# Kernel optimization log

Measured on AMD Instinct MI355X. Metric: run time of the kernel, lower is better.

## Reference

```python
import jax, jax.numpy as jnp
import numpy as np

B, C, N, K, CO = 16, 256, 16384, 64, 512
EPS_NORM = 1e-12
BN_EPS = 1e-5


def _l2norm(v, axis):
    n = jnp.sqrt(jnp.sum(v * v, axis=axis, keepdims=True))
    return v / jnp.maximum(n, EPS_NORM)


def setup_inputs() -> dict:
    key = jax.random.key(0)
    ks = jax.random.split(key, 8)
    x = jax.random.normal(ks[0], (B, C, N), dtype=jnp.float32)
    # NetVLAD assignment conv: Conv1d(C, K, k=1) -> weight (K, C), bias (K)
    assign_w = jax.random.normal(ks[1], (K, C), dtype=jnp.float32) / np.sqrt(C)
    assign_b = jax.random.normal(ks[2], (K,), dtype=jnp.float32) / np.sqrt(C)
    centroids = jax.random.uniform(ks[3], (K, C), dtype=jnp.float32)
    # reduct_feat Conv1d(K*C, CO, k=1): weight (CO, K*C), bias (CO)
    red_w = jax.random.normal(ks[4], (CO, K * C), dtype=jnp.float32) * np.sqrt(2.0 / (K * C))
    red_b = jnp.zeros((CO,), dtype=jnp.float32)
    bn_w = jnp.ones((CO,), dtype=jnp.float32)
    bn_b = jnp.zeros((CO,), dtype=jnp.float32)
    return {"x": x, "assign_w": assign_w, "assign_b": assign_b,
            "centroids": centroids, "red_w": red_w, "red_b": red_b,
            "bn_w": bn_w, "bn_b": bn_b}


def reference(x, assign_w, assign_b, centroids, red_w, red_b, bn_w, bn_b):
    # --- NetVLAD ---
    xn = _l2norm(x, axis=1)                                   # (B,C,N) L2 over channel
    logits = jnp.einsum('kc,bcn->bkn', assign_w, xn) + assign_b[None, :, None]
    a = jax.nn.softmax(logits, axis=1)                        # (B,K,N) soft assignment
    # residual aggregation reformulated: sum_n a*(x - c) = (a @ x^T) - sum_n(a) * c
    agg = jnp.einsum('bkn,bcn->bkc', a, xn)                   # (B,K,C)
    a_sum = jnp.sum(a, axis=2)                                # (B,K)
    vlad = agg - a_sum[:, :, None] * centroids[None, :, :]    # (B,K,C)
    vlad = _l2norm(vlad, axis=2)                              # intra-norm over C
    vlad = vlad.reshape(B, K * C)
    vlad = _l2norm(vlad, axis=1)                              # global L2
    # --- reduct_feat: 1x1 conv on length-1 sequence ---
    y = vlad @ red_w.T + red_b                                # (B,CO)
    # BatchNorm1d, training mode: stats over batch (L=1), biased variance
    mean = jnp.mean(y, axis=0)
    var = jnp.mean((y - mean) ** 2, axis=0)
    y = bn_w * (y - mean) / jnp.sqrt(var + BN_EPS) + bn_b
    y = jax.nn.relu(y)
    return y[:, :, None]                                      # (B,CO,1)
```

## Files before the change

### kernel.cpp

```cpp
#include <hip/hip_runtime.h>
#include <math.h>

#define B_   16
#define C_   256
#define N_   16384
#define K_   64
#define CO_  512

typedef __attribute__((ext_vector_type(8))) short short8;
typedef __attribute__((ext_vector_type(4))) short short4v;
typedef __attribute__((ext_vector_type(4))) float floatx4;

__device__ inline unsigned int f2bf(float f) {
    unsigned int u = __float_as_uint(f);
    return (u + 0x7FFFu + ((u >> 16) & 1u)) >> 16;
}


__global__ __launch_bounds__(512, 4) void k1_assign_agg(
    const float* __restrict__ x, const float* __restrict__ aw,
    const float* __restrict__ ab, float* __restrict__ agg,
    float* __restrict__ asum)
{
    __shared__ __align__(16) unsigned char smem[79872];
    unsigned short* x_cn = (unsigned short*)smem;
    unsigned short* x_nc = (unsigned short*)(smem + 32768);
    unsigned short* a_ld = (unsigned short*)(smem + 66048);
    float* colsq = (float*)(smem + 74240);
    float* rnorm = (float*)(smem + 78592);
    float* part  = (float*)(smem + 78848);
    float* red   = part;

    const int t    = threadIdx.x;
    const int lane = t & 63;
    const int wav  = t >> 6;
    const int b    = blockIdx.x >> 5;
    const int tile = blockIdx.x & 31;
    const float* xb = x + (size_t)b * ((size_t)C_ * N_) + tile * 512;

    const int j16 = lane & 15;
    const int g4  = lane >> 4;
    const int mw  = wav & 3;
    const int jw  = wav >> 2;
    const int p   = t & 31;
    const int g   = t >> 5;

    short8 wf[8];
    {
        const float* wrow = aw + (mw * 16 + j16) * 256 + g4 * 8;
        #pragma unroll
        for (int ki = 0; ki < 8; ++ki) {
            const float* q = wrow + ki * 32;
            short8 f;
            #pragma unroll
            for (int i = 0; i < 8; ++i) f[i] = (short)f2bf(q[i]);
            wf[ki] = f;
        }
    }
    const float4 abf = *(const float4*)(ab + mw * 16 + g4 * 4);

    floatx4 acc[4][2];
    #pragma unroll
    for (int m = 0; m < 4; ++m)
        #pragma unroll
        for (int c2 = 0; c2 < 2; ++c2)
            acc[m][c2] = (floatx4){0.f, 0.f, 0.f, 0.f};
    float asr[4] = {0.f, 0.f, 0.f, 0.f};

    float2 v[16];
    {
        const float* ps = xb + 2 * p;
        #pragma unroll
        for (int i = 0; i < 16; ++i)
            v[i] = *(const float2*)(ps + (size_t)(g * 16 + i) * N_);
    }

    for (int chunk = 0; chunk < 8; ++chunk) {
        __syncthreads();
        float sq0 = 0.f, sq1 = 0.f;
        #pragma unroll
        for (int half = 0; half < 2; ++half) {
            unsigned int hL[8], hH[8];
            #pragma unroll
            for (int i = 0; i < 8; ++i) {
                float2 vv = v[half * 8 + i];
                sq0 += vv.x * vv.x; sq1 += vv.y * vv.y;
                hL[i] = f2bf(vv.x); hH[i] = f2bf(vv.y);
                int c = g * 16 + half * 8 + i;
                ((unsigned int*)x_cn)[c * 32 + (((p >> 1) ^ (c & 14)) << 1) + (p & 1)]
                    = hL[i] | (hH[i] << 16);
            }
            unsigned short* r0 = x_nc + (2 * p) * 260 + g * 16 + half * 8;
            unsigned short* r1 = r0 + 260;
            uint2 wl0, wl1, wh0, wh1;
            wl0.x = hL[0] | (hL[1] << 16); wl0.y = hL[2] | (hL[3] << 16);
            wl1.x = hL[4] | (hL[5] << 16); wl1.y = hL[6] | (hL[7] << 16);
            wh0.x = hH[0] | (hH[1] << 16); wh0.y = hH[2] | (hH[3] << 16);
            wh1.x = hH[4] | (hH[5] << 16); wh1.y = hH[6] | (hH[7] << 16);
            *(uint2*)(r0 + 0) = wl0; *(uint2*)(r0 + 4) = wl1;
            *(uint2*)(r1 + 0) = wh0; *(uint2*)(r1 + 4) = wh1;
        }
        colsq[(2 * p) * 17 + g]     = sq0;
        colsq[(2 * p + 1) * 17 + g] = sq1;
        if (chunk < 7) {
            const float* ps = xb + (chunk + 1) * 64 + 2 * p;
            #pragma unroll
            for (int i = 0; i < 16; ++i)
                v[i] = *(const float2*)(ps + (size_t)(g * 16 + i) * N_);
        }
        __syncthreads();
        if (t < 64) {
            float s = 0.f;
            #pragma unroll
            for (int q = 0; q < 16; ++q) s += colsq[t * 17 + q];
            rnorm[t] = 1.0f / fmaxf(sqrtf(s), 1e-12f);
        }
        __syncthreads();
        floatx4 ct0 = {0.f, 0.f, 0.f, 0.f}, ct1 = {0.f, 0.f, 0.f, 0.f};
        {
            const unsigned short* rA0 = x_nc + (jw * 32 + j16) * 260 + g4 * 8;
            const unsigned short* rA1 = rA0 + 16 * 260;
            #pragma unroll
            for (int ki = 0; ki < 8; ++ki) {
                short4v a0 = *(const short4v*)(rA0 + ki * 32);
                short4v a1 = *(const short4v*)(rA0 + ki * 32 + 4);
                short4v b0 = *(const short4v*)(rA1 + ki * 32);
                short4v b1 = *(const short4v*)(rA1 + ki * 32 + 4);
                short8 f0, f1;
                #pragma unroll
                for (int i = 0; i < 4; ++i) {
                    f0[i] = a0[i]; f0[i + 4] = a1[i];
                    f1[i] = b0[i]; f1[i + 4] = b1[i];
                }
                ct0 = __builtin_amdgcn_mfma_f32_16x16x32_bf16(wf[ki], f0, ct0, 0, 0, 0);
                ct1 = __builtin_amdgcn_mfma_f32_16x16x32_bf16(wf[ki], f1, ct1, 0, 0, 0);
            }
        }
        const float rn0 = rnorm[jw * 32 + j16];
        const float rn1 = rnorm[jw * 32 + 16 + j16];
        float e0[4], e1[4];
        float p0 = 0.f, p1 = 0.f;
        #pragma unroll
        for (int r = 0; r < 4; ++r) {
            float l0 = ct0[r] * rn0 + ((const float*)&abf)[r];
            float l1 = ct1[r] * rn1 + ((const float*)&abf)[r];
            e0[r] = __expf(l0); e1[r] = __expf(l1);
            p0 += e0[r]; p1 += e1[r];
        }
        p0 += __shfl_xor(p0, 16); p0 += __shfl_xor(p0, 32);
        p1 += __shfl_xor(p1, 16); p1 += __shfl_xor(p1, 32);
        if (lane < 16) {
            part[(jw * 32 + j16) * 4 + mw]      = p0;
            part[(jw * 32 + 16 + j16) * 4 + mw] = p1;
        }
        __syncthreads();
        {
            float4 q0 = *(const float4*)(part + (jw * 32 + j16) * 4);
            float4 q1 = *(const float4*)(part + (jw * 32 + 16 + j16) * 4);
            float i0 = 1.0f / (q0.x + q0.y + q0.z + q0.w);
            float i1 = 1.0f / (q1.x + q1.y + q1.z + q1.w);
            float s0 = rn0 * i0, s1 = rn1 * i1;
            const int n0c = jw * 32 + j16, n1c = n0c + 16;
            #pragma unroll
            for (int r = 0; r < 4; ++r) {
                int k = mw * 16 + g4 * 4 + r;
                a_ld[k * 64 + ((((n0c) >> 2) ^ (k & 14)) << 2) + (n0c & 3)]
                    = (unsigned short)f2bf(e0[r] * s0);
                a_ld[k * 64 + ((((n1c) >> 2) ^ (k & 14)) << 2) + (n1c & 3)]
                    = (unsigned short)f2bf(e1[r] * s1);
                asr[r] += e0[r] * i0 + e1[r] * i1;
            }
        }
        __syncthreads();
        {
            const int cb = wav * 32;
            #pragma unroll
            for (int ki = 0; ki < 2; ++ki) {
                const int sub = ki * 8 + g4 * 2;
                short8 af[4];
                #pragma unroll
                for (int m = 0; m < 4; ++m) {
                    int k = m * 16 + j16;
                    af[m] = *(const short8*)&a_ld[k * 64 + ((sub ^ (k & 14)) << 2)];
                }
                #pragma unroll
                for (int c2 = 0; c2 < 2; ++c2) {
                    int c = cb + c2 * 16 + j16;
                    short8 bfv = *(const short8*)&x_cn[c * 64 + ((sub ^ (c & 14)) << 2)];
                    #pragma unroll
                    for (int m = 0; m < 4; ++m)
                        acc[m][c2] = __builtin_amdgcn_mfma_f32_16x16x32_bf16(af[m], bfv, acc[m][c2], 0, 0, 0);
                }
            }
        }
    }

    __syncthreads();
    #pragma unroll
    for (int r = 0; r < 4; ++r) {
        asr[r] += __shfl_xor(asr[r], 1);
        asr[r] += __shfl_xor(asr[r], 2);
        asr[r] += __shfl_xor(asr[r], 4);
        asr[r] += __shfl_xor(asr[r], 8);
    }
    if (j16 == 0) {
        #pragma unroll
        for (int r = 0; r < 4; ++r) red[wav * 16 + g4 * 4 + r] = asr[r];
    }
    __syncthreads();
    if (t < 64) {
        float s = red[(t >> 4) * 16 + (t & 15)] + red[((t >> 4) + 4) * 16 + (t & 15)];
        atomicAdd(&asum[b * 64 + t], s);
    }
    #pragma unroll
    for (int m = 0; m < 4; ++m)
        #pragma unroll
        for (int c2 = 0; c2 < 2; ++c2)
            #pragma unroll
            for (int r = 0; r < 4; ++r) {
                int k = m * 16 + g4 * 4 + r;
                int c = wav * 32 + c2 * 16 + j16;
                atomicAdd(&agg[((size_t)(b * 64 + k)) * 256 + c], acc[m][c2][r]);
            }
}

__global__ void k2a_vlad_norm(const float* __restrict__ agg,
                              const float* __restrict__ asum,
                              const float* __restrict__ cent,
                              float* __restrict__ vn,
                              float* __restrict__ gsq)
{
    const int b = blockIdx.x >> 6;
    const int k = blockIdx.x & 63;
    const int lane = threadIdx.x;
    const float as = asum[b * 64 + k];
    float v[4];
    float sq = 0.f;
    #pragma unroll
    for (int i = 0; i < 4; ++i) {
        int c = lane + 64 * i;
        v[i] = agg[((size_t)(b * 64 + k)) * 256 + c] - as * cent[k * 256 + c];
        sq += v[i] * v[i];
    }
    #pragma unroll
    for (int off = 32; off >= 1; off >>= 1) sq += __shfl_xor(sq, off);
    float scale = 1.0f / fmaxf(sqrtf(sq), 1e-12f);
    #pragma unroll
    for (int i = 0; i < 4; ++i) {
        int c = lane + 64 * i;
        vn[(size_t)b * 16384 + k * 256 + c] = v[i] * scale;
    }
    if (lane == 0) atomicAdd(&gsq[b], sq * scale * scale);
}

__global__ __launch_bounds__(256) void k2b_gemm(
    const float* __restrict__ vn, const float* __restrict__ rw,
    float* __restrict__ y)
{
    __shared__ float pr[4][16];
    const int t = threadIdx.x;
    const int co   = blockIdx.x >> 1;
    const int half = blockIdx.x & 1;
    const float4* rwr = (const float4*)rw + (size_t)co * 4096 + half * 2048;
    const float4* vnb = (const float4*)vn + half * 2048;
    float a0[16];
    #pragma unroll
    for (int bb = 0; bb < 16; ++bb) a0[bb] = 0.f;
    for (int it = 0; it < 8; ++it) {
        int idx = it * 256 + t;
        float4 w = rwr[idx];
        #pragma unroll
        for (int bb = 0; bb < 16; ++bb) {
            float4 vv = vnb[(size_t)bb * 4096 + idx];
            a0[bb] += w.x * vv.x + w.y * vv.y + w.z * vv.z + w.w * vv.w;
        }
    }
    #pragma unroll
    for (int off = 32; off >= 1; off >>= 1)
        #pragma unroll
        for (int bb = 0; bb < 16; ++bb)
            a0[bb] += __shfl_xor(a0[bb], off);
    const int wav = t >> 6, lane = t & 63;
    if (lane < 16) pr[wav][lane] = a0[lane];
    __syncthreads();
    if (t < 16)
        atomicAdd(&y[t * 512 + co], pr[0][t] + pr[1][t] + pr[2][t] + pr[3][t]);
}

__global__ void k2c_bn(const float* __restrict__ y,
                       const float* __restrict__ gsq,
                       const float* __restrict__ rb,
                       const float* __restrict__ bnw,
                       const float* __restrict__ bnb,
                       float* __restrict__ out)
{
    const int co = threadIdx.x;
    const float rbv = rb[co];
    float vals[16];
    float m = 0.f;
    #pragma unroll
    for (int bb = 0; bb < 16; ++bb) {
        float gv = fmaxf(sqrtf(gsq[bb]), 1e-12f);
        vals[bb] = y[bb * 512 + co] / gv + rbv;
        m += vals[bb];
    }
    m *= (1.0f / 16.0f);
    float var = 0.f;
    #pragma unroll
    for (int bb = 0; bb < 16; ++bb) {
        float d = vals[bb] - m;
        var += d * d;
    }
    var *= (1.0f / 16.0f);
    float inv = 1.0f / sqrtf(var + 1e-5f);
    float w = bnw[co], bias = bnb[co];
    #pragma unroll
    for (int bb = 0; bb < 16; ++bb) {
        float o = w * (vals[bb] - m) * inv + bias;
        out[bb * 512 + co] = fmaxf(o, 0.f);
    }
}

extern "C" void kernel_launch(void* const* d_in, const int* in_sizes, int n_in,
                              void* d_out, int out_size, void* d_ws, size_t ws_size,
                              hipStream_t stream)
{
    const float* x    = (const float*)d_in[0];
    const float* aw   = (const float*)d_in[1];
    const float* ab   = (const float*)d_in[2];
    const float* cent = (const float*)d_in[3];
    const float* rw   = (const float*)d_in[4];
    const float* rb   = (const float*)d_in[5];
    const float* bnw  = (const float*)d_in[6];
    const float* bnb  = (const float*)d_in[7];
    float* out = (float*)d_out;

    char* ws = (char*)d_ws;
    float* agg  = (float*)(ws);
    float* asum = (float*)(ws + 0x100000);
    float* gsq  = (float*)(ws + 0x101000);
    float* y    = (float*)(ws + 0x102000);
    float* vn   = (float*)(ws + 0x110000);

    hipMemsetAsync(ws, 0, 0x10A000, stream);

    hipLaunchKernelGGL(k1_assign_agg, dim3(512), dim3(512), 0, stream,
                       x, aw, ab, agg, asum);
    hipLaunchKernelGGL(k2a_vlad_norm, dim3(B_ * K_), dim3(64), 0, stream,
                       agg, asum, cent, vn, gsq);
    hipLaunchKernelGGL(k2b_gemm, dim3(CO_ * 2), dim3(256), 0, stream,
                       vn, rw, y);
    hipLaunchKernelGGL(k2c_bn, dim3(1), dim3(512), 0, stream,
                       y, gsq, rb, bnw, bnb, out);
}
```

Before: 523.5 us.

## Stage VLAD vectors in shared memory and reuse across eight outputs in reduction GEMM

The reduction GEMM now has each block handle 8 output channels over a quarter of the K*C dimension. It stages chunks of the 16 normalized VLAD rows into LDS so that all 8 channel groups reuse them, where before every block reread the VLAD vectors from global/L2. The grid shrinks from 1024 to 256 blocks, and each 32-lane group reduces its partials and atomically adds them to y. The assignment kernel's launch bounds are also rewritten as explicit amdgpu attributes that pin waves-per-EU to exactly 4. The added barriers, the ~66KB LDS footprint and the smaller grid may lower occupancy.

```diff
diff --git a/kernel.cpp b/kernel.cpp
--- a/kernel.cpp
+++ b/kernel.cpp
@@ -17,7 +17,9 @@
 }
 
 
-__global__ __launch_bounds__(512, 4) void k1_assign_agg(
+__global__ __attribute__((amdgpu_flat_work_group_size(512, 512),
+                          amdgpu_waves_per_eu(4, 4)))
+void k1_assign_agg(
     const float* __restrict__ x, const float* __restrict__ aw,
     const float* __restrict__ ab, float* __restrict__ agg,
     float* __restrict__ asum)
@@ -257,34 +259,50 @@
     const float* __restrict__ vn, const float* __restrict__ rw,
     float* __restrict__ y)
 {
-    __shared__ float pr[4][16];
-    const int t = threadIdx.x;
-    const int co   = blockIdx.x >> 1;
-    const int half = blockIdx.x & 1;
-    const float4* rwr = (const float4*)rw + (size_t)co * 4096 + half * 2048;
-    const float4* vnb = (const float4*)vn + half * 2048;
-    float a0[16];
-    #pragma unroll
-    for (int bb = 0; bb < 16; ++bb) a0[bb] = 0.f;
-    for (int it = 0; it < 8; ++it) {
-        int idx = it * 256 + t;
-        float4 w = rwr[idx];
+    __shared__ float vns[16][1032];
+    const int t   = threadIdx.x;
+    const int cg  = t >> 5;
+    const int tk  = t & 31;
+    const int cog = blockIdx.x >> 2;
+    const int kq  = blockIdx.x & 3;
+    const int co  = cog * 8 + cg;
+    const float4* vn4 = (const float4*)vn;
+    const float4* rw4 = (const float4*)rw;
+
+    float acc[16];
+    #pragma unroll
+    for (int bb = 0; bb < 16; ++bb) acc[bb] = 0.f;
+
+    for (int ch = 0; ch < 4; ++ch) {
+        const int kc4 = kq * 1024 + ch * 256;
+        __syncthreads();
         #pragma unroll
         for (int bb = 0; bb < 16; ++bb) {
-            float4 vv = vnb[(size_t)bb * 4096 + idx];
-            a0[bb] += w.x * vv.x + w.y * vv.y + w.z * vv.z + w.w * vv.w;
-        }
-    }
-    #pragma unroll
-    for (int off = 32; off >= 1; off >>= 1)
+            float4 vv = vn4[(size_t)bb * 4096 + kc4 + t];
+            *(float4*)&vns[bb][t << 2] = vv;
+        }
+        __syncthreads();
+        const float4* rwr = rw4 + (size_t)co * 4096 + kc4;
+        #pragma unroll
+        for (int j = 0; j < 8; ++j) {
+            float4 w = rwr[tk + 32 * j];
+            #pragma unroll
+            for (int bb = 0; bb < 16; ++bb) {
+                float4 vv = *(const float4*)&vns[bb][(tk + 32 * j) << 2];
+                acc[bb] += w.x * vv.x + w.y * vv.y + w.z * vv.z + w.w * vv.w;
+            }
+        }
+    }
+    #pragma unroll
+    for (int off = 16; off >= 1; off >>= 1)
         #pragma unroll
         for (int bb = 0; bb < 16; ++bb)
-            a0[bb] += __shfl_xor(a0[bb], off);
-    const int wav = t >> 6, lane = t & 63;
-    if (lane < 16) pr[wav][lane] = a0[lane];
-    __syncthreads();
-    if (t < 16)
-        atomicAdd(&y[t * 512 + co], pr[0][t] + pr[1][t] + pr[2][t] + pr[3][t]);
+            acc[bb] += __shfl_xor(acc[bb], off);
+    if (tk == 0) {
+        #pragma unroll
+        for (int bb = 0; bb < 16; ++bb)
+            atomicAdd(&y[bb * 512 + co], acc[bb]);
+    }
 }
 
 __global__ void k2c_bn(const float* __restrict__ y,
@@ -348,7 +366,7 @@
                        x, aw, ab, agg, asum);
     hipLaunchKernelGGL(k2a_vlad_norm, dim3(B_ * K_), dim3(64), 0, stream,
                        agg, asum, cent, vn, gsq);
-    hipLaunchKernelGGL(k2b_gemm, dim3(CO_ * 2), dim3(256), 0, stream,
+    hipLaunchKernelGGL(k2b_gemm, dim3(256), dim3(256), 0, stream,
                        vn, rw, y);
     hipLaunchKernelGGL(k2c_bn, dim3(1), dim3(512), 0, stream,
                        y, gsq, rb, bnw, bnb, out);
```

Measured after the change: 531.1 us. No clear change (+1.5%).
